# Optimization experiments

Measured on AMD Instinct MI355X. Metric: run time of the kernel, lower is better.

The kernel has to match this reference:

```python
import jax, jax.numpy as jnp
import numpy as np

B, T, CM, CZ, H = 2, 512, 256, 128, 16
DH = CM // H  # 16
EPS = 1e-5


def setup_inputs() -> dict:
    root = jax.random.key(0)
    ks = jax.random.split(root, 16)
    n = lambda i, shape: jax.random.normal(ks[i], shape, dtype=jnp.float32)
    s = np.float32(1.0 / np.sqrt(CM))
    return dict(
        query=n(0, (B, T, CM)),
        key=n(1, (B, T, CM)),
        value=n(2, (B, T, CM)),
        pos_embedding=n(3, (B, 2 * T - 1, CM)),  # T2 = 2T-1 relative positions
        z=n(4, (B, T, T, CZ)),
        mask=jax.random.randint(ks[5], (B, 1, T), 0, 2) > 0,
        Wq=n(6, (CM, CM)) * s, bq=jnp.zeros((CM,), jnp.float32),
        Wk=n(7, (CM, CM)) * s, bk=jnp.zeros((CM,), jnp.float32),
        Wv=n(8, (CM, CM)) * s, bv=jnp.zeros((CM,), jnp.float32),
        Wp=n(9, (CM, CM)) * s,
        u_bias=n(10, (H, DH)) * np.float32(0.1),
        v_bias=n(11, (H, DH)) * np.float32(0.1),
        Wo=n(12, (CM, CM)) * s, bo=jnp.zeros((CM,), jnp.float32),
        ln_g=jnp.ones((CZ,), jnp.float32), ln_b=jnp.zeros((CZ,), jnp.float32),
        Wz=n(13, (CZ, H)) * np.float32(1.0 / np.sqrt(CZ)),
    )


def _relative_shift(ps):
    # ps: (B, H, T1, T2) -> Transformer-XL relative shift, keep first T2//2+1 cols
    b, h, t1, t2 = ps.shape
    padded = jnp.pad(ps, ((0, 0), (0, 0), (0, 0), (1, 0)))  # (b,h,t1,t2+1)
    padded = padded.reshape(b, h, t2 + 1, t1)
    shifted = padded[:, :, 1:, :].reshape(b, h, t1, t2)
    return shifted[..., : t2 // 2 + 1]


def reference(query, key, value, pos_embedding, z, mask,
              Wq, bq, Wk, bk, Wv, bv, Wp, u_bias, v_bias, Wo, bo,
              ln_g, ln_b, Wz):
    b = query.shape[0]
    q = (query @ Wq.T + bq).reshape(b, -1, H, DH)          # (b,T,H,dh)
    k = (key @ Wk.T + bk).reshape(b, -1, H, DH)
    v = (value @ Wv.T + bv).reshape(b, -1, H, DH)
    p = (pos_embedding @ Wp.T).reshape(b, -1, H, DH)       # (b,2T-1,H,dh)

    content = jnp.einsum('bihd,bjhd->bhij', q + u_bias, k)     # (b,H,T,T)
    pos = jnp.einsum('bihd,bjhd->bhij', q + v_bias, p)         # (b,H,T,2T-1)
    pos = _relative_shift(pos)                                  # (b,H,T,T)

    # z bias: LayerNorm over c_z then project to heads (chunking in torch is a no-op math-wise)
    mu = jnp.mean(z, axis=-1, keepdims=True)
    var = jnp.var(z, axis=-1, keepdims=True)
    zn = (z - mu) * jax.lax.rsqrt(var + EPS) * ln_g + ln_b
    z_bias = jnp.einsum('bijc,ch->bhij', zn, Wz)                # (b,H,T,T)

    score = (content + pos) / np.float32(np.sqrt(DH)) + z_bias
    score = jnp.where(mask[:, None, :, :], jnp.float32(-10000.0), score)
    attn = jax.nn.softmax(score, axis=-1)  # dropout is identity in eval

    ctx = jnp.einsum('bhij,bjhd->bihd', attn, v).reshape(b, -1, CM)
    return ctx @ Wo.T + bo
```

## Files before the change

kernel.cpp:

```cpp
#include <hip/hip_runtime.h>
#include <hip/hip_bf16.h>

typedef __attribute__((ext_vector_type(8))) short short8;
typedef __attribute__((ext_vector_type(4))) short short4v;
typedef __attribute__((ext_vector_type(4))) float f32x4;

#define LD4(dst, v4) { dst[0]=(v4).x; dst[1]=(v4).y; dst[2]=(v4).z; dst[3]=(v4).w; }

static __device__ __forceinline__ short f2bf(float f) {
    union { float f; unsigned u; } v; v.f = f;
    unsigned r = (v.u + 0x7FFFu + ((v.u >> 16) & 1u)) >> 16;
    return (short)r;
}
static __device__ __forceinline__ float bf2f(short s) {
    union { unsigned u; float f; } v; v.u = ((unsigned)(unsigned short)s) << 16;
    return v.f;
}
static __device__ __forceinline__ unsigned cvt_pk_bf16(float lo, float hi) {
    unsigned r;
    asm volatile("v_cvt_pk_bf16_f32 %0, %1, %2" : "=v"(r) : "v"(lo), "v"(hi));
    return r;
}

static __device__ __forceinline__ void proj_tile(
    const float* __restrict__ X, const float* __restrict__ W,
    const float* __restrict__ bias, float* __restrict__ Yf,
    short* __restrict__ Yb, int M, int base, float* xs)
{
    int rt = base >> 1, ct = base & 1;
    int t = threadIdx.x;
    int row_base = rt * 32;
    {
        int r = t >> 3, k0 = (t & 7) * 32;
        int row = row_base + r;
        if (row < M) {
            const float* xp = X + (size_t)row * 256 + k0;
            #pragma unroll
            for (int q = 0; q < 8; ++q) {
                float4 v = *(const float4*)(xp + q * 4);
                xs[(k0 + q * 4 + 0) * 36 + r] = v.x;
                xs[(k0 + q * 4 + 1) * 36 + r] = v.y;
                xs[(k0 + q * 4 + 2) * 36 + r] = v.z;
                xs[(k0 + q * 4 + 3) * 36 + r] = v.w;
            }
        } else {
            #pragma unroll
            for (int q = 0; q < 32; ++q) xs[(k0 + q) * 36 + r] = 0.f;
        }
    }
    __syncthreads();
    int c_base = ct * 128 + (t & 31) * 4;
    int r_base = (t >> 5) * 4;
    float acc[4][4];
    #pragma unroll
    for (int a = 0; a < 4; ++a)
        #pragma unroll
        for (int b = 0; b < 4; ++b) acc[a][b] = 0.f;
    for (int k = 0; k < 256; k += 4) {
        float w0[4], w1[4], w2[4], w3[4];
        { float4 v = *(const float4*)(W + (size_t)(c_base + 0) * 256 + k); LD4(w0, v); }
        { float4 v = *(const float4*)(W + (size_t)(c_base + 1) * 256 + k); LD4(w1, v); }
        { float4 v = *(const float4*)(W + (size_t)(c_base + 2) * 256 + k); LD4(w2, v); }
        { float4 v = *(const float4*)(W + (size_t)(c_base + 3) * 256 + k); LD4(w3, v); }
        #pragma unroll
        for (int kk = 0; kk < 4; ++kk) {
            float xl[4];
            float4 xv = *(const float4*)(&xs[(k + kk) * 36 + r_base]);
            LD4(xl, xv);
            #pragma unroll
            for (int ri = 0; ri < 4; ++ri) {
                acc[ri][0] += xl[ri] * w0[kk];
                acc[ri][1] += xl[ri] * w1[kk];
                acc[ri][2] += xl[ri] * w2[kk];
                acc[ri][3] += xl[ri] * w3[kk];
            }
        }
    }
    #pragma unroll
    for (int ri = 0; ri < 4; ++ri) {
        int row = row_base + r_base + ri;
        if (row < M) {
            float o0 = acc[ri][0] + (bias ? bias[c_base + 0] : 0.f);
            float o1 = acc[ri][1] + (bias ? bias[c_base + 1] : 0.f);
            float o2 = acc[ri][2] + (bias ? bias[c_base + 2] : 0.f);
            float o3 = acc[ri][3] + (bias ? bias[c_base + 3] : 0.f);
            if (Yb) {
                short4v o; o[0] = f2bf(o0); o[1] = f2bf(o1); o[2] = f2bf(o2); o[3] = f2bf(o3);
                *(short4v*)(Yb + (size_t)row * 256 + c_base) = o;
            } else {
                float4 o; o.x = o0; o.y = o1; o.z = o2; o.w = o3;
                *(float4*)(Yf + (size_t)row * 256 + c_base) = o;
            }
        }
    }
}

__global__ void k_proj(const float* __restrict__ query, const float* __restrict__ key,
                       const float* __restrict__ value, const float* __restrict__ pos,
                       const float* __restrict__ Wq, const float* __restrict__ bq,
                       const float* __restrict__ Wk, const float* __restrict__ bk,
                       const float* __restrict__ Wv, const float* __restrict__ bv,
                       const float* __restrict__ Wp,
                       const float* __restrict__ ln_g, const float* __restrict__ ln_b,
                       const float* __restrict__ Wz, const int* __restrict__ mask,
                       float* __restrict__ qb, short* __restrict__ kbf,
                       short* __restrict__ vbf, short* __restrict__ pbf,
                       short* __restrict__ wzp, float* __restrict__ Ah, float* __restrict__ Ch,
                       int* __restrict__ idx, int* __restrict__ cnt)
{
    __shared__ float xs[256 * 36];
    int bx = blockIdx.x;
    if (bx == 320) {
        int lane = threadIdx.x & 63, wave = threadIdx.x >> 6;
        if (wave == 0) {
            for (int b = 0; b < 2; ++b) {
                int* idxb = idx + b * 512;
                #pragma unroll
                for (int q = 0; q < 8; ++q) idxb[q * 64 + lane] = -1;
                int total = 0;
                for (int q = 0; q < 8; ++q) {
                    int j = q * 64 + lane;
                    int u = (mask[b * 512 + j] == 0) ? 1 : 0;
                    unsigned long long bal = __ballot(u);
                    int p = total + __popcll(bal & ((1ull << lane) - 1ull));
                    if (u) idxb[p] = j;
                    total += (int)__popcll(bal);
                }
                if (total == 0) {
                    for (int q = 0; q < 8; ++q) idxb[q * 64 + lane] = q * 64 + lane;
                    total = 512;
                }
                if (lane == 0) cnt[b] = total;
            }
        } else if (wave == 1) {
            for (int id = lane; id < 2048; id += 64) {
                int m = id >> 9, rem = id & 511, l = rem >> 3, ii = rem & 7;
                int c = m * 32 + ((l >> 4) << 3) + ii, h = l & 15;
                wzp[id] = f2bf(ln_g[c] * Wz[c * 16 + h]);
            }
        } else if (wave == 2) {
            int h = lane & 15, part = lane >> 4;
            float a = 0.f, c = 0.f;
            #pragma unroll 4
            for (int cc = part * 32; cc < part * 32 + 32; ++cc) {
                float wv = Wz[cc * 16 + h];
                a += ln_g[cc] * wv;
                c += ln_b[cc] * wv;
            }
            a += __shfl_xor(a, 16); a += __shfl_xor(a, 32);
            c += __shfl_xor(c, 16); c += __shfl_xor(c, 32);
            if (part == 0) { Ah[h] = a; Ch[h] = c; }
        }
        return;
    }
    if (bx < 64)       proj_tile(query, Wq, bq, qb, nullptr, 1024, bx, xs);
    else if (bx < 128) proj_tile(key,   Wk, bk, nullptr, kbf, 1024, bx - 64, xs);
    else if (bx < 192) proj_tile(value, Wv, bv, nullptr, vbf, 1024, bx - 128, xs);
    else               proj_tile(pos,   Wp, nullptr, nullptr, pbf, 2046, bx - 192, xs);
}

__global__ void k_compact(const int* __restrict__ idx,
                          const short* __restrict__ kbf, const short* __restrict__ vbf,
                          short* __restrict__ kbfC, short* __restrict__ vbTC)
{
    __shared__ short st[32 * 264];
    const short8 z8v = {0,0,0,0,0,0,0,0};
    int bx = blockIdx.x;
    int b = bx >> 4, jn0 = (bx & 15) * 32;
    int t = threadIdx.x;
    int r = t >> 3, cc = (t & 7) * 32;
    int jn = jn0 + r;
    int jv = idx[b * 512 + jn];
    {
        short* dst = kbfC + ((size_t)b * 512 + jn) * 256 + cc;
        if (jv >= 0) {
            const short* src = kbf + ((size_t)b * 512 + jv) * 256 + cc;
            #pragma unroll
            for (int q = 0; q < 4; ++q) *(short8*)(dst + q * 8) = *(const short8*)(src + q * 8);
        } else {
            #pragma unroll
            for (int q = 0; q < 4; ++q) *(short8*)(dst + q * 8) = z8v;
        }
    }
    {
        if (jv >= 0) {
            const short* src = vbf + ((size_t)b * 512 + jv) * 256 + cc;
            #pragma unroll
            for (int q = 0; q < 4; ++q) *(short8*)(&st[r * 264 + cc + q * 8]) = *(const short8*)(src + q * 8);
        } else {
            #pragma unroll
            for (int q = 0; q < 4; ++q) *(short8*)(&st[r * 264 + cc + q * 8]) = z8v;
        }
        __syncthreads();
        int c = t;
        short tmp[32];
        #pragma unroll
        for (int q = 0; q < 32; ++q) tmp[q] = st[q * 264 + c];
        short* dst = vbTC + ((size_t)b * 256 + c) * 512 + jn0;
        #pragma unroll
        for (int q = 0; q < 4; ++q) *(short8*)(dst + q * 8) = *(const short8*)(&tmp[q * 8]);
    }
}

__global__ void __launch_bounds__(256, 3) k_attn_z(
    const float* __restrict__ z,
    const float* __restrict__ qb, const short* __restrict__ kbfC, const short* __restrict__ pbf,
    const short* __restrict__ wzp, const float* __restrict__ Ah, const float* __restrict__ Ch,
    const float* __restrict__ u_bias, const float* __restrict__ v_bias,
    const int* __restrict__ idx, const int* __restrict__ cnt,
    const short* __restrict__ vbTC,
    const float* __restrict__ Wo, const float* __restrict__ bo, float* __restrict__ out)
{
    __shared__ __align__(16) char lds_raw[35072];
    short* zs_all = (short*)lds_raw;
    short* wT   = (short*)(lds_raw + 16896);
    float* redm = (float*)(lds_raw + 33536);
    float* reds = (float*)(lds_raw + 33792);
    float* ctxl = (float*)(lds_raw + 34048);
    const short8 zero8 = {0, 0, 0, 0, 0, 0, 0, 0};

    int bi = blockIdx.x;
    int b = bi >> 9, i = bi & 511;
    int t = threadIdx.x;
    int lane = t & 63, wave = t >> 6;
    int h = lane & 15, g = lane >> 4;
    int l5 = lane >> 5, l31 = lane & 31;
    int np = (min(cnt[b], 512) + 31) & ~31;
    int nt16 = np >> 4;
    short* zs = zs_all + wave * 2112;
    const float* zb_ = z + (size_t)bi * 65536;

    short8 wz[4];
    #pragma unroll
    for (int m = 0; m < 4; ++m) wz[m] = *(const short8*)(wzp + m * 512 + lane * 8);
    float ah = Ah[h], ch = Ch[h];

    bool act = ((h & 1) == (g >> 1));
    int m_act = act ? (h >> 1) : 8;
    short8 qu8 = zero8, qv8 = zero8;
    {
        int c0q = h * 16 + (g & 1) * 8;
        const float* qp = qb + (size_t)bi * 256 + c0q;
        #pragma unroll
        for (int ii = 0; ii < 8; ++ii) {
            float qv_ = qp[ii];
            qu8[ii] = f2bf(0.25f * (qv_ + u_bias[c0q + ii]));
            qv8[ii] = f2bf(0.25f * (qv_ + v_bias[c0q + ii]));
        }
        if (!act) { qu8 = zero8; qv8 = zero8; }
    }

    int idxq[8];
    #pragma unroll
    for (int q = 0; q < 8; ++q) {
        int tl = wave + q * 4;
        idxq[q] = (tl < nt16) ? idx[b * 512 + tl * 16 + h] : -1;
    }

    f32x4 sc[8];
    float mloc = -3.0e38f;
    #pragma unroll
    for (int q = 0; q < 8; ++q) {
        int tl = wave + q * 4;
        if (tl < nt16) {
            float4 zv[8];
            #pragma unroll
            for (int m = 0; m < 8; ++m) {
                int r = 2 * m + l5;
                int jv = __shfl(idxq[q], r);
                int jr = (jv < 0) ? 0 : jv;
                zv[m] = *(const float4*)(zb_ + (size_t)jr * 128 + l31 * 4);
            }
            int jn = tl * 16 + h;
            int jvh = idxq[q];
            int jrp = 511 + ((jvh < 0) ? 0 : jvh) - i;
            const short* kr = kbfC + ((size_t)b * 512 + jn) * 256 + g * 8;
            const short* pr = pbf + ((size_t)b * 1023 + jrp) * 256 + g * 8;
            f32x4 acp = {0.f, 0.f, 0.f, 0.f};
            #pragma unroll
            for (int m = 0; m < 8; ++m) {
                short8 ka = *(const short8*)(kr + m * 32);
                short8 pa = *(const short8*)(pr + m * 32);
                short8 bu = (m == m_act) ? qu8 : zero8;
                short8 bv = (m == m_act) ? qv8 : zero8;
                acp = __builtin_amdgcn_mfma_f32_16x16x32_bf16(ka, bu, acp, 0, 0, 0);
                acp = __builtin_amdgcn_mfma_f32_16x16x32_bf16(pa, bv, acp, 0, 0, 0);
            }
            #pragma unroll
            for (int m = 0; m < 8; ++m) {
                int r = 2 * m + l5;
                uint2 pk;
                pk.x = cvt_pk_bf16(zv[m].x, zv[m].y);
                pk.y = cvt_pk_bf16(zv[m].z, zv[m].w);
                *(uint2*)(&zs[r * 132 + l31 * 4]) = pk;
            }
            short8 af[4];
            float sum = 0.f, sq = 0.f;
            #pragma unroll
            for (int m = 0; m < 4; ++m) {
                short4v a0 = *(const short4v*)(&zs[h * 132 + g * 8 + m * 32]);
                short4v a1 = *(const short4v*)(&zs[h * 132 + g * 8 + m * 32 + 4]);
                short8 s8;
                s8[0] = a0[0]; s8[1] = a0[1]; s8[2] = a0[2]; s8[3] = a0[3];
                s8[4] = a1[0]; s8[5] = a1[1]; s8[6] = a1[2]; s8[7] = a1[3];
                af[m] = s8;
                #pragma unroll
                for (int ii = 0; ii < 8; ++ii) {
                    float x = bf2f(s8[ii]);
                    sum += x;
                    sq = fmaf(x, x, sq);
                }
            }
            sum += __shfl_xor(sum, 16); sum += __shfl_xor(sum, 32);
            sq  += __shfl_xor(sq, 16);  sq  += __shfl_xor(sq, 32);
            float mu = sum * (1.f / 128.f);
            float rs = rsqrtf(sq * (1.f / 128.f) - mu * mu + 1e-5f);
            f32x4 accz = {0.f, 0.f, 0.f, 0.f};
            #pragma unroll
            for (int m = 0; m < 4; ++m)
                accz = __builtin_amdgcn_mfma_f32_16x16x32_bf16(af[m], wz[m], accz, 0, 0, 0);
            int4 jv4 = *(const int4*)(idx + b * 512 + tl * 16 + g * 4);
            int jj4[4]; jj4[0] = jv4.x; jj4[1] = jv4.y; jj4[2] = jv4.z; jj4[3] = jv4.w;
            #pragma unroll
            for (int reg = 0; reg < 4; ++reg) {
                int orow = g * 4 + reg;
                float mo = __shfl(mu, orow);
                float ro = __shfl(rs, orow);
                float s = acp[reg] + ro * (accz[reg] - mo * ah) + ch;
                s = (jj4[reg] < 0) ? -3.0e38f : s;
                sc[q][reg] = s;
                mloc = fmaxf(mloc, s);
            }
        }
    }

    mloc = fmaxf(mloc, __shfl_xor(mloc, 16));
    mloc = fmaxf(mloc, __shfl_xor(mloc, 32));
    redm[wave * 16 + h] = mloc;
    __syncthreads();
    float mg = fmaxf(fmaxf(redm[h], redm[16 + h]), fmaxf(redm[32 + h], redm[48 + h]));
    float ssum = 0.f;
    #pragma unroll
    for (int q = 0; q < 8; ++q) {
        int tl = wave + q * 4;
        if (tl < nt16) {
            #pragma unroll
            for (int reg = 0; reg < 4; ++reg) {
                float e = __expf(sc[q][reg] - mg);
                sc[q][reg] = e;
                ssum += e;
            }
        }
    }
    ssum += __shfl_xor(ssum, 16); ssum += __shfl_xor(ssum, 32);
    reds[wave * 16 + h] = ssum;
    __syncthreads();
    float sg = reds[h] + reds[16 + h] + reds[32 + h] + reds[48 + h];
    float inv = 1.f / sg;
    #pragma unroll
    for (int q = 0; q < 8; ++q) {
        int tl = wave + q * 4;
        if (tl < nt16) {
            short4v w4;
            #pragma unroll
            for (int reg = 0; reg < 4; ++reg) w4[reg] = f2bf(sc[q][reg] * inv);
            *(short4v*)(&wT[h * 520 + tl * 16 + g * 4]) = w4;
        }
    }
    __syncthreads();

    #pragma unroll
    for (int q = 0; q < 4; ++q) {
        int hp = wave * 4 + q;
        int c0 = hp * 16;
        const short* vrow = vbTC + ((size_t)b * 256 + c0 + h) * 512;
        f32x4 a0 = {0.f, 0.f, 0.f, 0.f};
        for (int jn0 = 0; jn0 < np; jn0 += 32) {
            short8 wA = *(const short8*)(&wT[hp * 520 + jn0 + g * 8]);
            short8 vB = *(const short8*)(vrow + jn0 + g * 8);
            a0 = __builtin_amdgcn_mfma_f32_16x16x32_bf16(wA, vB, a0, 0, 0, 0);
        }
        if (g == 0) ctxl[c0 + h] = a0[0];
    }
    __syncthreads();

    {
        float acc = bo[t];
        const float* wrow = Wo + (size_t)t * 256;
        #pragma unroll 4
        for (int k = 0; k < 256; k += 8) {
            float4 w0 = *(const float4*)(wrow + k);
            float4 w1 = *(const float4*)(wrow + k + 4);
            acc += ctxl[k + 0] * w0.x + ctxl[k + 1] * w0.y
                 + ctxl[k + 2] * w0.z + ctxl[k + 3] * w0.w
                 + ctxl[k + 4] * w1.x + ctxl[k + 5] * w1.y
                 + ctxl[k + 6] * w1.z + ctxl[k + 7] * w1.w;
        }
        out[(size_t)bi * 256 + t] = acc;
    }
}

extern "C" void kernel_launch(void* const* d_in, const int* in_sizes, int n_in,
                              void* d_out, int out_size, void* d_ws, size_t ws_size,
                              hipStream_t stream) {
    const float* query = (const float*)d_in[0];
    const float* key   = (const float*)d_in[1];
    const float* value = (const float*)d_in[2];
    const float* pos   = (const float*)d_in[3];
    const float* z     = (const float*)d_in[4];
    const int*   mask  = (const int*)d_in[5];
    const float* Wq = (const float*)d_in[6];
    const float* bq = (const float*)d_in[7];
    const float* Wk = (const float*)d_in[8];
    const float* bk = (const float*)d_in[9];
    const float* Wv = (const float*)d_in[10];
    const float* bv = (const float*)d_in[11];
    const float* Wp = (const float*)d_in[12];
    const float* u_bias = (const float*)d_in[13];
    const float* v_bias = (const float*)d_in[14];
    const float* Wo = (const float*)d_in[15];
    const float* bo = (const float*)d_in[16];
    const float* ln_g = (const float*)d_in[17];
    const float* ln_b = (const float*)d_in[18];
    const float* Wz = (const float*)d_in[19];

    char* ws = (char*)d_ws;
    float* qb   = (float*)(ws + 0);
    short* kbf  = (short*)(ws + (1u << 20));
    short* vbf  = (short*)(ws + 1572864u);
    short* pbf  = (short*)(ws + (2u << 20));
    short* wzp  = (short*)(ws + (3u << 20));
    float* Ah   = (float*)(ws + (3u << 20) + 4096);
    float* Ch   = (float*)(ws + (3u << 20) + 4160);
    int*   idx  = (int*)(ws + (3u << 20) + 8192);
    int*   cnt  = (int*)(ws + (3u << 20) + 16384);
    short* kbfC = (short*)(ws + (4u << 20));
    short* vbTC = (short*)(ws + 4718592u);

    hipLaunchKernelGGL(k_proj, dim3(321), dim3(256), 0, stream,
                       query, key, value, pos, Wq, bq, Wk, bk, Wv, bv, Wp,
                       ln_g, ln_b, Wz, mask,
                       qb, kbf, vbf, pbf, wzp, Ah, Ch, idx, cnt);
    hipLaunchKernelGGL(k_compact, dim3(32), dim3(256), 0, stream,
                       idx, kbf, vbf, kbfC, vbTC);
    hipLaunchKernelGGL(k_attn_z, dim3(1024), dim3(256), 0, stream,
                       z, qb, kbfC, pbf, wzp, Ah, Ch, u_bias, v_bias, idx, cnt, vbTC,
                       Wo, bo, (float*)d_out);
}
```

Measured before the change: 179.6 us.

## Load z rows directly into MFMA fragments, drop LDS staging, reorder blocks

Each lane now reads its 8-float slices of the gathered z row straight into registers in MFMA A-fragment layout. LayerNorm statistics are computed in fp32 before the bf16 pack, so the LDS round trip and the bf16 re-read are gone and shared memory shrinks from about 35KB to 18KB. The block index is permuted across groups of 8 blocks to change scheduling locality, and s_setprio is raised around the MFMA loops. The mask value now comes from a shuffle of idxq instead of a second global load. Per-lane reads become 32-byte strided segments rather than fully coalesced 512-byte rows, which may change memory efficiency.

```diff
diff --git a/kernel.cpp b/kernel.cpp
--- a/kernel.cpp
+++ b/kernel.cpp
@@ -11,10 +11,6 @@
     union { float f; unsigned u; } v; v.f = f;
     unsigned r = (v.u + 0x7FFFu + ((v.u >> 16) & 1u)) >> 16;
     return (short)r;
-}
-static __device__ __forceinline__ float bf2f(short s) {
-    union { unsigned u; float f; } v; v.u = ((unsigned)(unsigned short)s) << 16;
-    return v.f;
 }
 static __device__ __forceinline__ unsigned cvt_pk_bf16(float lo, float hi) {
     unsigned r;
@@ -211,23 +207,20 @@
     const short* __restrict__ vbTC,
     const float* __restrict__ Wo, const float* __restrict__ bo, float* __restrict__ out)
 {
-    __shared__ __align__(16) char lds_raw[35072];
-    short* zs_all = (short*)lds_raw;
-    short* wT   = (short*)(lds_raw + 16896);
-    float* redm = (float*)(lds_raw + 33536);
-    float* reds = (float*)(lds_raw + 33792);
-    float* ctxl = (float*)(lds_raw + 34048);
+    __shared__ __align__(16) char lds_raw[18176];
+    short* wT   = (short*)lds_raw;
+    float* redm = (float*)(lds_raw + 16640);
+    float* reds = (float*)(lds_raw + 16896);
+    float* ctxl = (float*)(lds_raw + 17152);
     const short8 zero8 = {0, 0, 0, 0, 0, 0, 0, 0};
 
-    int bi = blockIdx.x;
+    int bi = (blockIdx.x & 7) * 128 + (blockIdx.x >> 3);
     int b = bi >> 9, i = bi & 511;
     int t = threadIdx.x;
     int lane = t & 63, wave = t >> 6;
     int h = lane & 15, g = lane >> 4;
-    int l5 = lane >> 5, l31 = lane & 31;
     int np = (min(cnt[b], 512) + 31) & ~31;
     int nt16 = np >> 4;
-    short* zs = zs_all + wave * 2112;
     const float* zb_ = z + (size_t)bi * 65536;
 
     short8 wz[4];
@@ -263,20 +256,21 @@
     for (int q = 0; q < 8; ++q) {
         int tl = wave + q * 4;
         if (tl < nt16) {
-            float4 zv[8];
-            #pragma unroll
-            for (int m = 0; m < 8; ++m) {
-                int r = 2 * m + l5;
-                int jv = __shfl(idxq[q], r);
-                int jr = (jv < 0) ? 0 : jv;
-                zv[m] = *(const float4*)(zb_ + (size_t)jr * 128 + l31 * 4);
+            int jvh = idxq[q];
+            int jr = (jvh < 0) ? 0 : jvh;
+            const float* zr = zb_ + (size_t)jr * 128 + g * 8;
+            float4 za0[4], za1[4];
+            #pragma unroll
+            for (int m = 0; m < 4; ++m) {
+                za0[m] = *(const float4*)(zr + m * 32);
+                za1[m] = *(const float4*)(zr + m * 32 + 4);
             }
             int jn = tl * 16 + h;
-            int jvh = idxq[q];
-            int jrp = 511 + ((jvh < 0) ? 0 : jvh) - i;
+            int jrp = 511 + jr - i;
             const short* kr = kbfC + ((size_t)b * 512 + jn) * 256 + g * 8;
             const short* pr = pbf + ((size_t)b * 1023 + jrp) * 256 + g * 8;
             f32x4 acp = {0.f, 0.f, 0.f, 0.f};
+            __builtin_amdgcn_s_setprio(1);
             #pragma unroll
             for (int m = 0; m < 8; ++m) {
                 short8 ka = *(const short8*)(kr + m * 32);
@@ -286,48 +280,42 @@
                 acp = __builtin_amdgcn_mfma_f32_16x16x32_bf16(ka, bu, acp, 0, 0, 0);
                 acp = __builtin_amdgcn_mfma_f32_16x16x32_bf16(pa, bv, acp, 0, 0, 0);
             }
-            #pragma unroll
-            for (int m = 0; m < 8; ++m) {
-                int r = 2 * m + l5;
-                uint2 pk;
-                pk.x = cvt_pk_bf16(zv[m].x, zv[m].y);
-                pk.y = cvt_pk_bf16(zv[m].z, zv[m].w);
-                *(uint2*)(&zs[r * 132 + l31 * 4]) = pk;
-            }
+            __builtin_amdgcn_s_setprio(0);
+            float sum = 0.f, sq = 0.f;
             short8 af[4];
-            float sum = 0.f, sq = 0.f;
             #pragma unroll
             for (int m = 0; m < 4; ++m) {
-                short4v a0 = *(const short4v*)(&zs[h * 132 + g * 8 + m * 32]);
-                short4v a1 = *(const short4v*)(&zs[h * 132 + g * 8 + m * 32 + 4]);
-                short8 s8;
-                s8[0] = a0[0]; s8[1] = a0[1]; s8[2] = a0[2]; s8[3] = a0[3];
-                s8[4] = a1[0]; s8[5] = a1[1]; s8[6] = a1[2]; s8[7] = a1[3];
-                af[m] = s8;
-                #pragma unroll
-                for (int ii = 0; ii < 8; ++ii) {
-                    float x = bf2f(s8[ii]);
-                    sum += x;
-                    sq = fmaf(x, x, sq);
-                }
+                sum += za0[m].x + za0[m].y + za0[m].z + za0[m].w
+                     + za1[m].x + za1[m].y + za1[m].z + za1[m].w;
+                sq = fmaf(za0[m].x, za0[m].x, sq); sq = fmaf(za0[m].y, za0[m].y, sq);
+                sq = fmaf(za0[m].z, za0[m].z, sq); sq = fmaf(za0[m].w, za0[m].w, sq);
+                sq = fmaf(za1[m].x, za1[m].x, sq); sq = fmaf(za1[m].y, za1[m].y, sq);
+                sq = fmaf(za1[m].z, za1[m].z, sq); sq = fmaf(za1[m].w, za1[m].w, sq);
+                union { short8 s; uint4 u; } pk;
+                pk.u.x = cvt_pk_bf16(za0[m].x, za0[m].y);
+                pk.u.y = cvt_pk_bf16(za0[m].z, za0[m].w);
+                pk.u.z = cvt_pk_bf16(za1[m].x, za1[m].y);
+                pk.u.w = cvt_pk_bf16(za1[m].z, za1[m].w);
+                af[m] = pk.s;
             }
             sum += __shfl_xor(sum, 16); sum += __shfl_xor(sum, 32);
             sq  += __shfl_xor(sq, 16);  sq  += __shfl_xor(sq, 32);
             float mu = sum * (1.f / 128.f);
             float rs = rsqrtf(sq * (1.f / 128.f) - mu * mu + 1e-5f);
             f32x4 accz = {0.f, 0.f, 0.f, 0.f};
+            __builtin_amdgcn_s_setprio(1);
             #pragma unroll
             for (int m = 0; m < 4; ++m)
                 accz = __builtin_amdgcn_mfma_f32_16x16x32_bf16(af[m], wz[m], accz, 0, 0, 0);
-            int4 jv4 = *(const int4*)(idx + b * 512 + tl * 16 + g * 4);
-            int jj4[4]; jj4[0] = jv4.x; jj4[1] = jv4.y; jj4[2] = jv4.z; jj4[3] = jv4.w;
+            __builtin_amdgcn_s_setprio(0);
             #pragma unroll
             for (int reg = 0; reg < 4; ++reg) {
                 int orow = g * 4 + reg;
                 float mo = __shfl(mu, orow);
                 float ro = __shfl(rs, orow);
+                int jj = __shfl(idxq[q], orow);
                 float s = acp[reg] + ro * (accz[reg] - mo * ah) + ch;
-                s = (jj4[reg] < 0) ? -3.0e38f : s;
+                s = (jj < 0) ? -3.0e38f : s;
                 sc[q][reg] = s;
                 mloc = fmaxf(mloc, s);
             }
@@ -375,11 +363,13 @@
         int c0 = hp * 16;
         const short* vrow = vbTC + ((size_t)b * 256 + c0 + h) * 512;
         f32x4 a0 = {0.f, 0.f, 0.f, 0.f};
+        __builtin_amdgcn_s_setprio(1);
         for (int jn0 = 0; jn0 < np; jn0 += 32) {
             short8 wA = *(const short8*)(&wT[hp * 520 + jn0 + g * 8]);
             short8 vB = *(const short8*)(vrow + jn0 + g * 8);
             a0 = __builtin_amdgcn_mfma_f32_16x16x32_bf16(wA, vB, a0, 0, 0, 0);
         }
+        __builtin_amdgcn_s_setprio(0);
         if (g == 0) ctxl[c0 + h] = a0[0];
     }
     __syncthreads();
```

New measurement: 249.8 us. 39.1% more time.
